# Optimization experiments

Measured on AMD Instinct MI355X. Metric: run time of the kernel, lower is better.

Reference implementation:

```python
import jax, jax.numpy as jnp
import numpy as np

B, N, NVT, HS = 512, 32, 32, 501
VS = HS + N  # vid=True: hidden state concat one-hot vertex id


def _init(key, shape, scale=0.05):
    return scale * jax.random.normal(key, shape, dtype=jnp.float32)


def setup_inputs() -> dict:
    key = jax.random.key(0)
    ks = jax.random.split(key, 12)
    node_types = jax.random.randint(ks[0], (B, N), 0, NVT)
    raw = jax.random.uniform(ks[1], (B, N, N))
    adj = (raw < 0.15).astype(jnp.float32) * jnp.triu(jnp.ones((N, N), jnp.float32), 1)
    return dict(
        node_types=node_types,
        adj=adj,
        Wg=_init(ks[2], (HS, VS)), bg=_init(ks[3], (HS,)),
        Wm=_init(ks[4], (HS, VS)),
        W_ih=_init(ks[5], (3 * HS, NVT)), b_ih=_init(ks[6], (3 * HS,)),
        W_hh=_init(ks[7], (3 * HS, HS)), b_hh=_init(ks[8], (3 * HS,)),
        W_reg=_init(ks[9], (N, HS)), b_reg=_init(ks[10], (N,)),
    )


def reference(node_types, adj, Wg, bg, Wm, W_ih, b_ih, W_hh, b_hh, W_reg, b_reg):
    x = jax.nn.one_hot(node_types, NVT, dtype=jnp.float32)          # [B,N,nvt]
    ids = jnp.broadcast_to(jnp.eye(N, dtype=jnp.float32), (B, N, N))  # vertex-id one-hots

    def gru(xv, h):  # torch.nn.GRUCell semantics, gate order r,z,n
        gi = xv @ W_ih.T + b_ih
        gh = h @ W_hh.T + b_hh
        ir, iz, i_n = jnp.split(gi, 3, axis=-1)
        hr, hz, h_n = jnp.split(gh, 3, axis=-1)
        r = jax.nn.sigmoid(ir + hr)
        z = jax.nn.sigmoid(iz + hz)
        n = jnp.tanh(i_n + r * h_n)
        return (1.0 - z) * n + z * h

    def step(H_all, inp):
        v, xv, pred = inp  # xv:[B,nvt], pred:[B,N] predecessor mask of vertex v
        Hcat = jnp.concatenate([H_all, ids], axis=-1)  # [B,N,VS]
        # gate(h)*mapper(h); mapper has no bias so padded/uncomputed rows give 0
        gated = jax.nn.sigmoid(jnp.einsum('buv,hv->buh', Hcat, Wg) + bg) \
                * jnp.einsum('buv,hv->buh', Hcat, Wm)  # [B,N,HS]
        Hmsg = jnp.einsum('bu,buh->bh', pred, gated)   # sum over predecessors
        Hv = gru(xv, Hmsg)
        return H_all.at[:, v, :].set(Hv), None

    H0 = jnp.zeros((B, N, HS), jnp.float32)
    xs = (jnp.arange(N), jnp.swapaxes(x, 0, 1), jnp.moveaxis(adj, 2, 0))
    H_all, _ = jax.lax.scan(step, H0, xs)
    Hg = H_all[:, N - 1]                 # graph state = last vertex's hidden
    mu = Hg @ W_reg.T + b_reg
    return mu
```

## Files before the change

kernel.cpp:

```cpp
#include <hip/hip_runtime.h>

#define BATCH 512
#define NN    32
#define NVT   32
#define HS    501
#define VS    533
#define KP    512

typedef short bf16x8 __attribute__((ext_vector_type(8)));
typedef float f32x4  __attribute__((ext_vector_type(4)));

__device__ __forceinline__ unsigned short f2bf(float f) {
    unsigned int u = __float_as_uint(f);
    u += 0x7fffu + ((u >> 16) & 1u);
    return (unsigned short)(u >> 16);
}
__device__ __forceinline__ float bf2f(unsigned short s) {
    return __uint_as_float(((unsigned int)s) << 16);
}
__device__ __forceinline__ float sigmoidf_(float x) { return 1.0f / (1.0f + __expf(-x)); }
__device__ __forceinline__ float tanhf_(float x)    { return 1.0f - 2.0f / (1.0f + __expf(2.0f * x)); }

#define N_WHH  (3 * KP * KP)
#define N_WGM  (2 * KP * KP)
#define N_GI   (3 * NVT * KP)
#define N_IDW  (2 * NN * KP)
#define N_WRT  (KP * NN)
#define N_MSGB (BATCH * KP)
#define N_ADJC (BATCH * NN)
#define N_TOT  (N_WHH + N_WGM + N_GI + N_IDW + N_WRT + N_MSGB + N_ADJC)

#define CB_WORDS (16 + 8 * 512 + 8 * 16)

__global__ void prep_kernel(const float* __restrict__ W_hh, const float* __restrict__ Wg,
                            const float* __restrict__ Wm, const float* __restrict__ W_ih,
                            const float* __restrict__ b_ih, const float* __restrict__ b_hh,
                            const float* __restrict__ bg, const float* __restrict__ W_reg,
                            const float* __restrict__ adj,
                            unsigned short* __restrict__ Whh_p, unsigned short* __restrict__ Wgm_p,
                            float* __restrict__ gi_tab, float* __restrict__ idw,
                            float* __restrict__ WregT, unsigned short* __restrict__ MsgB,
                            unsigned int* __restrict__ adjcG)
{
    for (int i = blockIdx.x * blockDim.x + threadIdx.x; i < N_TOT; i += gridDim.x * blockDim.x) {
        int j = i;
        if (j < N_WHH) {
            int g = j >> 18, rem = j & (KP * KP - 1);
            int h = rem >> 9, k = rem & (KP - 1);
            float val = 0.0f;
            if (h < HS) {
                if (k < HS)        val = W_hh[(size_t)(g * HS + h) * HS + k];
                else if (k == HS)  val = b_hh[g * HS + h];
            }
            Whh_p[j] = f2bf(val);
            continue;
        }
        j -= N_WHH;
        if (j < N_WGM) {
            int m = j >> 18, rem = j & (KP * KP - 1);
            int h = rem >> 9, k = rem & (KP - 1);
            const float* src = m ? Wm : Wg;
            Wgm_p[j] = (h < HS && k < HS) ? f2bf(src[(size_t)h * VS + k]) : (unsigned short)0;
            continue;
        }
        j -= N_WGM;
        if (j < N_GI) {
            int g = j >> 14, typ = (j >> 9) & 31, h = j & (KP - 1);
            gi_tab[j] = (h < HS) ? (W_ih[(size_t)(g * HS + h) * NVT + typ] + b_ih[g * HS + h]) : 0.0f;
            continue;
        }
        j -= N_GI;
        if (j < N_IDW) {
            int m = j >> 14, v = (j >> 9) & 31, h = j & (KP - 1);
            float val = 0.0f;
            if (h < HS)
                val = m ? Wm[(size_t)h * VS + HS + v]
                        : (Wg[(size_t)h * VS + HS + v] + bg[h]);
            idw[j] = val;
            continue;
        }
        j -= N_IDW;
        if (j < N_WRT) {
            int k = j >> 5, ii = j & 31;
            WregT[j] = (k < HS) ? W_reg[(size_t)ii * HS + k] : 0.0f;
            continue;
        }
        j -= N_WRT;
        if (j < N_MSGB) {
            int k = j & (KP - 1);
            MsgB[j] = (k == HS) ? (unsigned short)0x3F80 : (unsigned short)0;
            continue;
        }
        j -= N_MSGB;
        {
            int b = j >> 5, vp = j & 31;
            unsigned int bits = 0;
            #pragma unroll
            for (int u = 0; u < 32; u++)
                bits |= (adj[((size_t)b * NN + u) * NN + vp] != 0.0f ? 1u : 0u) << u;
            adjcG[j] = bits;
        }
    }
}

__device__ __forceinline__ void sbar(unsigned int* flags, unsigned int* rel,
                                     int slot, unsigned int ph) {
    __syncthreads();
    const int t = threadIdx.x;
    if (t < 64) {
        if (t == 0)
            __hip_atomic_store(&flags[slot * 16], ph, __ATOMIC_RELAXED,
                               __HIP_MEMORY_SCOPE_AGENT);
        if (slot == 0) {
            unsigned long long notready;
            do {
                const unsigned int fv = (t < 32)
                    ? __hip_atomic_load(&flags[t * 16], __ATOMIC_RELAXED,
                                        __HIP_MEMORY_SCOPE_AGENT)
                    : ph;
                notready = __ballot(fv < ph);
                if (notready) __builtin_amdgcn_s_sleep(2);
            } while (notready);
            if (t == 0)
                __hip_atomic_store(rel, ph, __ATOMIC_RELAXED, __HIP_MEMORY_SCOPE_AGENT);
        } else if (t == 0) {
            while (__hip_atomic_load(rel, __ATOMIC_RELAXED, __HIP_MEMORY_SCOPE_AGENT) < ph)
                __builtin_amdgcn_s_sleep(2);
        }
    }
    __syncthreads();
}

__global__ __launch_bounds__(512, 1) void dvae_kernel(
    const unsigned short* __restrict__ Whh,
    const unsigned short* __restrict__ Wgm,
    const float* __restrict__ gi_tab,
    const float* __restrict__ idw,
    const int*   __restrict__ types,
    const unsigned int* __restrict__ adjcG,
    unsigned short* __restrict__ MsgB,
    unsigned short* __restrict__ HvB,
    unsigned short* __restrict__ Ghist,
    float* __restrict__ HvF,
    unsigned int* __restrict__ cb)
{
    __shared__ unsigned short WLDS[80 * 512];
    __shared__ float          Cred[12 * 256];
    __shared__ float          MsgF_L[64 * 16];
    __shared__ unsigned short GvL[64 * 16];
    __shared__ unsigned int   adjcL[64 * 32];
    __shared__ int            slotS;

    int xcd;
    asm volatile("s_getreg_b32 %0, hwreg(HW_REG_XCC_ID)" : "=s"(xcd));
    xcd &= 7;
    if (threadIdx.x == 0)
        slotS = (int)__hip_atomic_fetch_add(&cb[xcd], 1u, __ATOMIC_RELAXED,
                                            __HIP_MEMORY_SCOPE_AGENT);
    __syncthreads();
    const int slot = slotS;
    if (slot >= 32) return;
    const int hblk = slot, bslc = xcd;
    unsigned int* flags = cb + 16 + (bslc << 9);
    unsigned int* rel   = cb + 16 + 4096 + (bslc << 4);

    const int t    = threadIdx.x;
    const int lane = t & 63, w = t >> 6;
    const int c16  = lane & 15, kg = lane >> 4;
    const int bt   = w & 3, kh = w >> 2;

    for (int i = 0; i < 10; i++) {
        const int seg = i * 512 + t;
        const int R = seg >> 6, k8 = (seg & 63) * 8;
        const unsigned short* src;
        if (R < 48) {
            const int g = R >> 4, r = R & 15;
            src = Whh + (((size_t)(g * 512 + hblk * 16 + r)) << 9) + k8;
        } else {
            const int m = (R - 48) >> 4, r = (R - 48) & 15;
            src = Wgm + (((size_t)(m * 512 + hblk * 16 + r)) << 9) + k8;
        }
        const bf16x8 val = *(const bf16x8*)src;
        const int didx = ((R << 10) + (k8 << 1)) ^ ((R & 7) << 4);
        *(bf16x8*)&WLDS[didx >> 1] = val;
    }
    for (int i = t; i < 64 * 32; i += 512) adjcL[i] = adjcG[bslc * (64 * 32) + i];
    for (int i = t; i < 64 * 16; i += 512) MsgF_L[i] = 0.0f;
    __syncthreads();

    unsigned short* Gblk = Ghist + (size_t)(bslc * 32 + hblk) * (32 * 64 * 16);
    unsigned int ph = 0;

    for (int v = 0; v < NN; v++) {
        f32x4 a0 = {0.f,0.f,0.f,0.f}, a1 = a0, a2 = a0;
        {
            const volatile unsigned short* aptr =
                MsgB + (((size_t)(bslc * 64 + bt * 16 + c16)) << 9) + kh * 256 + kg * 8;
            const int wi0 = (((c16 << 10) + ((kh * 256 + kg * 8) << 1)) ^ ((c16 & 7) << 4)) >> 1;
            const int wi1 = wi0 + 8192, wi2 = wi0 + 16384;
            #pragma unroll
            for (int kk = 0; kk < 8; kk++) {
                const bf16x8 af = *(const volatile bf16x8*)(aptr + kk * 32);
                a0 = __builtin_amdgcn_mfma_f32_16x16x32_bf16(af, *(const bf16x8*)&WLDS[wi0 ^ (kk*32)], a0, 0, 0, 0);
                a1 = __builtin_amdgcn_mfma_f32_16x16x32_bf16(af, *(const bf16x8*)&WLDS[wi1 ^ (kk*32)], a1, 0, 0, 0);
                a2 = __builtin_amdgcn_mfma_f32_16x16x32_bf16(af, *(const bf16x8*)&WLDS[wi2 ^ (kk*32)], a2, 0, 0, 0);
            }
        }
        if (kh == 1) {
            #pragma unroll
            for (int j = 0; j < 4; j++) {
                const int pi = (kg * 4 + j) * 16 + c16;
                Cred[(bt * 3 + 0) * 256 + pi] = a0[j];
                Cred[(bt * 3 + 1) * 256 + pi] = a1[j];
                Cred[(bt * 3 + 2) * 256 + pi] = a2[j];
            }
        }
        __syncthreads();
        if (kh == 0) {
            const int h = hblk * 16 + c16;
            const bool ok = (h < HS);
            #pragma unroll
            for (int j = 0; j < 4; j++) {
                const int pi = (kg * 4 + j) * 16 + c16;
                const float s0 = a0[j] + Cred[(bt * 3 + 0) * 256 + pi];
                const float s1 = a1[j] + Cred[(bt * 3 + 1) * 256 + pi];
                const float s2 = a2[j] + Cred[(bt * 3 + 2) * 256 + pi];
                const int bl = bt * 16 + kg * 4 + j;
                const int bg_ = bslc * 64 + bl;
                float hv = 0.0f;
                if (ok) {
                    const int typ = types[bg_ * 32 + v];
                    const float gr = gi_tab[(0 * 32 + typ) * 512 + h];
                    const float gz = gi_tab[(1 * 32 + typ) * 512 + h];
                    const float gn = gi_tab[(2 * 32 + typ) * 512 + h];
                    const float hmsg = MsgF_L[bl * 16 + c16];
                    const float r = sigmoidf_(gr + s0);
                    const float z = sigmoidf_(gz + s1);
                    const float n = tanhf_(gn + r * s2);
                    hv = (1.0f - z) * n + z * hmsg;
                }
                HvB[((size_t)bg_ << 9) + h] = f2bf(hv);
                if (v == NN - 1) HvF[((size_t)bg_ << 9) + h] = hv;
            }
        }
        if (v == NN - 1) break;
        sbar(flags, rel, hblk, ++ph);

        f32x4 b0 = {0.f,0.f,0.f,0.f}, b1 = b0;
        {
            const volatile unsigned short* aptr =
                HvB + (((size_t)(bslc * 64 + bt * 16 + c16)) << 9) + kh * 256 + kg * 8;
            const int wi0 = ((((48 + c16) << 10) + ((kh * 256 + kg * 8) << 1)) ^ ((c16 & 7) << 4)) >> 1;
            const int wi1 = wi0 + 8192;
            #pragma unroll
            for (int kk = 0; kk < 8; kk++) {
                const bf16x8 af = *(const volatile bf16x8*)(aptr + kk * 32);
                b0 = __builtin_amdgcn_mfma_f32_16x16x32_bf16(af, *(const bf16x8*)&WLDS[wi0 ^ (kk*32)], b0, 0, 0, 0);
                b1 = __builtin_amdgcn_mfma_f32_16x16x32_bf16(af, *(const bf16x8*)&WLDS[wi1 ^ (kk*32)], b1, 0, 0, 0);
            }
        }
        if (kh == 1) {
            #pragma unroll
            for (int j = 0; j < 4; j++) {
                const int pi = (kg * 4 + j) * 16 + c16;
                Cred[(bt * 2 + 0) * 256 + pi] = b0[j];
                Cred[(bt * 2 + 1) * 256 + pi] = b1[j];
            }
        }
        __syncthreads();
        if (kh == 0) {
            const int h = hblk * 16 + c16;
            const bool ok = (h < HS);
            #pragma unroll
            for (int j = 0; j < 4; j++) {
                const int pi = (kg * 4 + j) * 16 + c16;
                const float s0 = b0[j] + Cred[(bt * 2 + 0) * 256 + pi];
                const float s1 = b1[j] + Cred[(bt * 2 + 1) * 256 + pi];
                const int bl = bt * 16 + kg * 4 + j;
                float gq = 0.0f;
                if (ok) {
                    const float zg = s0 + idw[(0 * 32 + v) * 512 + h];
                    const float zm = s1 + idw[(1 * 32 + v) * 512 + h];
                    gq = sigmoidf_(zg) * zm;
                }
                GvL[bl * 16 + c16] = f2bf(gq);
            }
        }
        __syncthreads();
        if (t < 128) {
            const int bl = t >> 1, h8 = (t & 1) * 8;
            const bf16x8 g = *(const bf16x8*)&GvL[bl * 16 + h8];
            *(bf16x8*)&Gblk[((size_t)v * 64 + bl) * 16 + h8] = g;

            float msg[8] = {0.f,0.f,0.f,0.f,0.f,0.f,0.f,0.f};
            unsigned int mask = adjcL[bl * 32 + (v + 1)] & ((2u << v) - 1u);
            if ((mask >> v) & 1u) {
                #pragma unroll
                for (int x = 0; x < 8; x++) msg[x] += bf2f((unsigned short)g[x]);
                mask &= ~(1u << v);
            }
            while (mask) {
                const int u = __builtin_ctz(mask); mask &= mask - 1u;
                const bf16x8 a = *(const bf16x8*)&Gblk[((size_t)u * 64 + bl) * 16 + h8];
                #pragma unroll
                for (int x = 0; x < 8; x++) msg[x] += bf2f((unsigned short)a[x]);
            }
            const int hb_ = hblk * 16 + h8;
            if (hb_ <= HS && HS < hb_ + 8) msg[HS - hb_] = 1.0f;
            bf16x8 mb;
            #pragma unroll
            for (int x = 0; x < 8; x++) mb[x] = (short)f2bf(msg[x]);
            *(bf16x8*)&MsgB[(((size_t)(bslc * 64 + bl)) << 9) + hb_] = mb;
            #pragma unroll
            for (int x = 0; x < 8; x++) MsgF_L[bl * 16 + h8 + x] = msg[x];
        }
        sbar(flags, rel, hblk, ++ph);
    }
}

__global__ __launch_bounds__(256) void final_kernel(
    const float* __restrict__ HvF,
    const float* __restrict__ WregT,
    const float* __restrict__ b_reg,
    float* __restrict__ out)
{
    const int t = blockIdx.x * 256 + threadIdx.x;
    const int b = t >> 5, i = t & 31;
    float s = b_reg[i];
    const float* hp = HvF + ((size_t)b << 9);
    #pragma unroll 4
    for (int k = 0; k < KP; k++) s += hp[k] * WregT[k * 32 + i];
    out[b * 32 + i] = s;
}

extern "C" void kernel_launch(void* const* d_in, const int* in_sizes, int n_in,
                              void* d_out, int out_size, void* d_ws, size_t ws_size,
                              hipStream_t stream) {
    const int*   node_types = (const int*)  d_in[0];
    const float* adj        = (const float*)d_in[1];
    const float* Wg         = (const float*)d_in[2];
    const float* bg         = (const float*)d_in[3];
    const float* Wm         = (const float*)d_in[4];
    const float* W_ih       = (const float*)d_in[5];
    const float* b_ih       = (const float*)d_in[6];
    const float* W_hh       = (const float*)d_in[7];
    const float* b_hh       = (const float*)d_in[8];
    const float* W_reg      = (const float*)d_in[9];
    const float* b_reg      = (const float*)d_in[10];
    float* out = (float*)d_out;

    char* p = (char*)d_ws;
    unsigned short* Whh_p = (unsigned short*)p; p += (size_t)N_WHH * 2;
    unsigned short* Wgm_p = (unsigned short*)p; p += (size_t)N_WGM * 2;
    float* gi_tab = (float*)p; p += (size_t)N_GI * 4;
    float* idw    = (float*)p; p += (size_t)N_IDW * 4;
    float* WregT  = (float*)p; p += (size_t)N_WRT * 4;
    float* HvF    = (float*)p; p += (size_t)BATCH * KP * 4;
    unsigned short* MsgB = (unsigned short*)p; p += (size_t)N_MSGB * 2;
    unsigned short* HvB  = (unsigned short*)p; p += (size_t)BATCH * KP * 2;
    unsigned int* adjcG  = (unsigned int*)p;  p += (size_t)N_ADJC * 4;
    unsigned int* cb     = (unsigned int*)p;  p += (size_t)CB_WORDS * 4;
    unsigned short* Ghist = (unsigned short*)p; p += (size_t)256 * 32 * 64 * 16 * 2;

    hipMemsetAsync(cb, 0, CB_WORDS * 4, stream);
    prep_kernel<<<1024, 256, 0, stream>>>(W_hh, Wg, Wm, W_ih, b_ih, b_hh, bg, W_reg, adj,
                                          Whh_p, Wgm_p, gi_tab, idw, WregT, MsgB, adjcG);
    dvae_kernel<<<1024, 512, 0, stream>>>(Whh_p, Wgm_p, gi_tab, idw, node_types, adjcG,
                                          MsgB, HvB, Ghist, HvF, cb);
    final_kernel<<<(BATCH * NN) / 256, 256, 0, stream>>>(HvF, WregT, b_reg, out);
}
```

Measured before the change: 396.6 us.

## Split K reduction across four wave groups with 1024-thread blocks

The persistent recurrence kernel now uses 1024 threads per block, so each wave handles a quarter of the K dimension (4 MFMA k-steps) instead of half. Partial sums from three wave groups go through a larger LDS reduction buffer. The weight tile in LDS is relaid out into MFMA-fragment order, which removes the XOR swizzle arithmetic. This is meant to shorten the serial per-step MFMA chain in the latency-bound recurrence. The cost is more LDS reduction traffic and heavier barriers across 16 waves, and __launch_bounds__(1024,4) may squeeze registers.

```diff
diff --git a/kernel.cpp b/kernel.cpp
--- a/kernel.cpp
+++ b/kernel.cpp
@@ -131,7 +131,7 @@
     __syncthreads();
 }
 
-__global__ __launch_bounds__(512, 1) void dvae_kernel(
+__global__ __launch_bounds__(1024, 4) void dvae_kernel(
     const unsigned short* __restrict__ Whh,
     const unsigned short* __restrict__ Wgm,
     const float* __restrict__ gi_tab,
@@ -144,8 +144,8 @@
     float* __restrict__ HvF,
     unsigned int* __restrict__ cb)
 {
-    __shared__ unsigned short WLDS[80 * 512];
-    __shared__ float          Cred[12 * 256];
+    __shared__ unsigned short WLDS[5 * 8192];
+    __shared__ float          Cred[3 * 12 * 256];
     __shared__ float          MsgF_L[64 * 16];
     __shared__ unsigned short GvL[64 * 16];
     __shared__ unsigned int   adjcL[64 * 32];
@@ -168,24 +168,21 @@
     const int lane = t & 63, w = t >> 6;
     const int c16  = lane & 15, kg = lane >> 4;
     const int bt   = w & 3, kh = w >> 2;
-
-    for (int i = 0; i < 10; i++) {
-        const int seg = i * 512 + t;
-        const int R = seg >> 6, k8 = (seg & 63) * 8;
-        const unsigned short* src;
-        if (R < 48) {
-            const int g = R >> 4, r = R & 15;
-            src = Whh + (((size_t)(g * 512 + hblk * 16 + r)) << 9) + k8;
-        } else {
-            const int m = (R - 48) >> 4, r = (R - 48) & 15;
-            src = Wgm + (((size_t)(m * 512 + hblk * 16 + r)) << 9) + k8;
-        }
-        const bf16x8 val = *(const bf16x8*)src;
-        const int didx = ((R << 10) + (k8 << 1)) ^ ((R & 7) << 4);
-        *(bf16x8*)&WLDS[didx >> 1] = val;
+    const int lofs = lane * 8;
+
+    {
+        const int kkf = t >> 6, l = t & 63;
+        const int r16 = l & 15, k0 = (l >> 4) * 8 + kkf * 32;
+        #pragma unroll
+        for (int T = 0; T < 5; T++) {
+            const unsigned short* src = (T < 3)
+                ? Whh + (((size_t)(T * 512 + hblk * 16 + r16)) << 9) + k0
+                : Wgm + (((size_t)((T - 3) * 512 + hblk * 16 + r16)) << 9) + k0;
+            *(bf16x8*)&WLDS[T * 8192 + kkf * 512 + l * 8] = *(const bf16x8*)src;
+        }
     }
-    for (int i = t; i < 64 * 32; i += 512) adjcL[i] = adjcG[bslc * (64 * 32) + i];
-    for (int i = t; i < 64 * 16; i += 512) MsgF_L[i] = 0.0f;
+    for (int i = t; i < 64 * 32; i += 1024) adjcL[i] = adjcG[bslc * (64 * 32) + i];
+    for (int i = t; i < 64 * 16; i += 1024) MsgF_L[i] = 0.0f;
     __syncthreads();
 
     unsigned short* Gblk = Ghist + (size_t)(bslc * 32 + hblk) * (32 * 64 * 16);
@@ -195,24 +192,23 @@
         f32x4 a0 = {0.f,0.f,0.f,0.f}, a1 = a0, a2 = a0;
         {
             const volatile unsigned short* aptr =
-                MsgB + (((size_t)(bslc * 64 + bt * 16 + c16)) << 9) + kh * 256 + kg * 8;
-            const int wi0 = (((c16 << 10) + ((kh * 256 + kg * 8) << 1)) ^ ((c16 & 7) << 4)) >> 1;
-            const int wi1 = wi0 + 8192, wi2 = wi0 + 16384;
-            #pragma unroll
-            for (int kk = 0; kk < 8; kk++) {
+                MsgB + (((size_t)(bslc * 64 + bt * 16 + c16)) << 9) + kh * 128 + kg * 8;
+            #pragma unroll
+            for (int kk = 0; kk < 4; kk++) {
                 const bf16x8 af = *(const volatile bf16x8*)(aptr + kk * 32);
-                a0 = __builtin_amdgcn_mfma_f32_16x16x32_bf16(af, *(const bf16x8*)&WLDS[wi0 ^ (kk*32)], a0, 0, 0, 0);
-                a1 = __builtin_amdgcn_mfma_f32_16x16x32_bf16(af, *(const bf16x8*)&WLDS[wi1 ^ (kk*32)], a1, 0, 0, 0);
-                a2 = __builtin_amdgcn_mfma_f32_16x16x32_bf16(af, *(const bf16x8*)&WLDS[wi2 ^ (kk*32)], a2, 0, 0, 0);
-            }
-        }
-        if (kh == 1) {
+                const int wo = (kh * 4 + kk) * 512 + lofs;
+                a0 = __builtin_amdgcn_mfma_f32_16x16x32_bf16(af, *(const bf16x8*)&WLDS[0 * 8192 + wo], a0, 0, 0, 0);
+                a1 = __builtin_amdgcn_mfma_f32_16x16x32_bf16(af, *(const bf16x8*)&WLDS[1 * 8192 + wo], a1, 0, 0, 0);
+                a2 = __builtin_amdgcn_mfma_f32_16x16x32_bf16(af, *(const bf16x8*)&WLDS[2 * 8192 + wo], a2, 0, 0, 0);
+            }
+        }
+        if (kh > 0) {
             #pragma unroll
             for (int j = 0; j < 4; j++) {
                 const int pi = (kg * 4 + j) * 16 + c16;
-                Cred[(bt * 3 + 0) * 256 + pi] = a0[j];
-                Cred[(bt * 3 + 1) * 256 + pi] = a1[j];
-                Cred[(bt * 3 + 2) * 256 + pi] = a2[j];
+                Cred[((kh - 1) * 12 + bt * 3 + 0) * 256 + pi] = a0[j];
+                Cred[((kh - 1) * 12 + bt * 3 + 1) * 256 + pi] = a1[j];
+                Cred[((kh - 1) * 12 + bt * 3 + 2) * 256 + pi] = a2[j];
             }
         }
         __syncthreads();
@@ -222,9 +218,15 @@
             #pragma unroll
             for (int j = 0; j < 4; j++) {
                 const int pi = (kg * 4 + j) * 16 + c16;
-                const float s0 = a0[j] + Cred[(bt * 3 + 0) * 256 + pi];
-                const float s1 = a1[j] + Cred[(bt * 3 + 1) * 256 + pi];
-                const float s2 = a2[j] + Cred[(bt * 3 + 2) * 256 + pi];
+                const float s0 = a0[j] + Cred[(0 * 12 + bt * 3 + 0) * 256 + pi]
+                                       + Cred[(1 * 12 + bt * 3 + 0) * 256 + pi]
+                                       + Cred[(2 * 12 + bt * 3 + 0) * 256 + pi];
+                const float s1 = a1[j] + Cred[(0 * 12 + bt * 3 + 1) * 256 + pi]
+                                       + Cred[(1 * 12 + bt * 3 + 1) * 256 + pi]
+                                       + Cred[(2 * 12 + bt * 3 + 1) * 256 + pi];
+                const float s2 = a2[j] + Cred[(0 * 12 + bt * 3 + 2) * 256 + pi]
+                                       + Cred[(1 * 12 + bt * 3 + 2) * 256 + pi]
+                                       + Cred[(2 * 12 + bt * 3 + 2) * 256 + pi];
                 const int bl = bt * 16 + kg * 4 + j;
                 const int bg_ = bslc * 64 + bl;
                 float hv = 0.0f;
@@ -249,22 +251,21 @@
         f32x4 b0 = {0.f,0.f,0.f,0.f}, b1 = b0;
         {
             const volatile unsigned short* aptr =
-                HvB + (((size_t)(bslc * 64 + bt * 16 + c16)) << 9) + kh * 256 + kg * 8;
-            const int wi0 = ((((48 + c16) << 10) + ((kh * 256 + kg * 8) << 1)) ^ ((c16 & 7) << 4)) >> 1;
-            const int wi1 = wi0 + 8192;
-            #pragma unroll
-            for (int kk = 0; kk < 8; kk++) {
+                HvB + (((size_t)(bslc * 64 + bt * 16 + c16)) << 9) + kh * 128 + kg * 8;
+            #pragma unroll
+            for (int kk = 0; kk < 4; kk++) {
                 const bf16x8 af = *(const volatile bf16x8*)(aptr + kk * 32);
-                b0 = __builtin_amdgcn_mfma_f32_16x16x32_bf16(af, *(const bf16x8*)&WLDS[wi0 ^ (kk*32)], b0, 0, 0, 0);
-                b1 = __builtin_amdgcn_mfma_f32_16x16x32_bf16(af, *(const bf16x8*)&WLDS[wi1 ^ (kk*32)], b1, 0, 0, 0);
-            }
-        }
-        if (kh == 1) {
+                const int wo = (kh * 4 + kk) * 512 + lofs;
+                b0 = __builtin_amdgcn_mfma_f32_16x16x32_bf16(af, *(const bf16x8*)&WLDS[3 * 8192 + wo], b0, 0, 0, 0);
+                b1 = __builtin_amdgcn_mfma_f32_16x16x32_bf16(af, *(const bf16x8*)&WLDS[4 * 8192 + wo], b1, 0, 0, 0);
+            }
+        }
+        if (kh > 0) {
             #pragma unroll
             for (int j = 0; j < 4; j++) {
                 const int pi = (kg * 4 + j) * 16 + c16;
-                Cred[(bt * 2 + 0) * 256 + pi] = b0[j];
-                Cred[(bt * 2 + 1) * 256 + pi] = b1[j];
+                Cred[((kh - 1) * 12 + bt * 3 + 0) * 256 + pi] = b0[j];
+                Cred[((kh - 1) * 12 + bt * 3 + 1) * 256 + pi] = b1[j];
             }
         }
         __syncthreads();
@@ -274,8 +275,12 @@
             #pragma unroll
             for (int j = 0; j < 4; j++) {
                 const int pi = (kg * 4 + j) * 16 + c16;
-                const float s0 = b0[j] + Cred[(bt * 2 + 0) * 256 + pi];
-                const float s1 = b1[j] + Cred[(bt * 2 + 1) * 256 + pi];
+                const float s0 = b0[j] + Cred[(0 * 12 + bt * 3 + 0) * 256 + pi]
+                                       + Cred[(1 * 12 + bt * 3 + 0) * 256 + pi]
+                                       + Cred[(2 * 12 + bt * 3 + 0) * 256 + pi];
+                const float s1 = b1[j] + Cred[(0 * 12 + bt * 3 + 1) * 256 + pi]
+                                       + Cred[(1 * 12 + bt * 3 + 1) * 256 + pi]
+                                       + Cred[(2 * 12 + bt * 3 + 1) * 256 + pi];
                 const int bl = bt * 16 + kg * 4 + j;
                 float gq = 0.0f;
                 if (ok) {
@@ -365,7 +370,7 @@
     hipMemsetAsync(cb, 0, CB_WORDS * 4, stream);
     prep_kernel<<<1024, 256, 0, stream>>>(W_hh, Wg, Wm, W_ih, b_ih, b_hh, bg, W_reg, adj,
                                           Whh_p, Wgm_p, gi_tab, idw, WregT, MsgB, adjcG);
-    dvae_kernel<<<1024, 512, 0, stream>>>(Whh_p, Wgm_p, gi_tab, idw, node_types, adjcG,
-                                          MsgB, HvB, Ghist, HvF, cb);
+    dvae_kernel<<<1024, 1024, 0, stream>>>(Whh_p, Wgm_p, gi_tab, idw, node_types, adjcG,
+                                           MsgB, HvB, Ghist, HvF, cb);
     final_kernel<<<(BATCH * NN) / 256, 256, 0, stream>>>(HvF, WregT, b_reg, out);
 }
```

Measured after the change: 401.3 us. About the same (+1.2%).
